# Performance work log

Measured on AMD Instinct MI355X. Metric: run time of the kernel, lower is better.

## Reference

```python
import jax, jax.numpy as jnp
import numpy as np

GROUP_SIZE = 64  # int4 precision
QMAX = 7.0       # symmetric int4 quant scale divisor


def setup_inputs() -> dict:
    key = jax.random.key(0)
    ks = jax.random.split(key, 8)
    B, S, C_in, C_out, R = 1, 4096, 3072, 3072, 32
    G = C_in // GROUP_SIZE
    x = jax.random.normal(ks[0], (B, S, C_in), dtype=jnp.float32)
    # unpacked int4 weight codes in [0,16); reference subtracts 8 -> signed int4 [-8,7]
    qweight = jax.random.randint(ks[1], (C_out, C_in), 0, 16, dtype=jnp.int32)
    # small positive per-group, per-out-channel weight scales
    wscales = jax.random.uniform(ks[2], (G, C_out), dtype=jnp.float32) * 0.01 + 0.001
    # positive smoothing factors bounded away from zero
    smooth_factor = jax.random.uniform(ks[3], (C_in,), dtype=jnp.float32) + 0.5
    proj_down = jax.random.normal(ks[4], (C_in, R), dtype=jnp.float32) * (1.0 / np.sqrt(C_in))
    proj_up = jax.random.normal(ks[5], (C_out, R), dtype=jnp.float32) * (1.0 / np.sqrt(R))
    bias = jax.random.normal(ks[6], (C_out,), dtype=jnp.float32) * 0.02
    return {
        "x": x,
        "qweight": qweight,
        "wscales": wscales,
        "smooth_factor": smooth_factor,
        "proj_down": proj_down,
        "proj_up": proj_up,
        "bias": bias,
    }


def reference(x, qweight, wscales, smooth_factor, proj_down, proj_up, bias):
    B, S, C = x.shape
    C_out = qweight.shape[0]
    M = B * S
    G = C // GROUP_SIZE

    # --- smoothing: x_hat = x / s (SVDQuant smoothing on activations) ---
    xs = x.reshape(M, C) / smooth_factor  # (M, C)

    # --- low-rank branch hidden state (fused with quantization in CUDA kernel) ---
    lora_act = jnp.einsum('mc,cr->mr', xs, proj_down)  # (M, R)

    # --- dynamic per-token, per-group int4 activation quantization ---
    xg = xs.reshape(M, G, GROUP_SIZE)
    amax = jnp.max(jnp.abs(xg), axis=-1, keepdims=True)          # (M, G, 1)
    ascale = amax / QMAX
    q = jnp.clip(jnp.round(xg / jnp.maximum(ascale, 1e-8)), -8.0, 7.0)
    x_dq = (q * ascale).reshape(M, C)                            # dequantized activations

    # --- weight dequantization: signed int4 codes * per-group/out-channel scales ---
    qw = qweight.astype(jnp.float32) - 8.0                       # (C_out, C) in [-8, 7]
    w_dq = (qw.reshape(C_out, G, GROUP_SIZE) * wscales.T[:, :, None]).reshape(C_out, C)

    # --- quantized GEMM + low-rank correction + bias ---
    out = jnp.einsum('mc,oc->mo', x_dq, w_dq)
    out = out + jnp.einsum('mr,or->mo', lora_act, proj_up) + bias
    return out.reshape(B, S, C_out)
```

## Files before the change

### kernel.cpp

```cpp
#include <hip/hip_runtime.h>
#include <stdint.h>

typedef unsigned short u16;

#define MTOK 4096
#define CIN  3072
#define COUT 3072
#define RANK 32
#define KT48 48
#define RS   3136
#define LKSPLIT 16
#define LKC (CIN/LKSPLIT)

#define LORA_BLK (MTOK/128*LKSPLIT)
#define WDQ_BLK COUT


typedef __attribute__((ext_vector_type(8))) short bf16x8;
typedef __attribute__((ext_vector_type(4))) float f32x4;

__device__ __forceinline__ u16 f2bf(float f) {
  union { float f; unsigned u; } v; v.f = f;
  unsigned r = v.u + 0x7FFFu + ((v.u >> 16) & 1u);
  return (u16)(r >> 16);
}

__device__ __forceinline__ void gload_lds16(const void* g, void* l) {
  __builtin_amdgcn_global_load_lds(
      (const __attribute__((address_space(1))) unsigned int*)g,
      (__attribute__((address_space(3))) unsigned int*)l, 16, 0, 0);
}

__device__ __forceinline__ float quant1(float xs, float ascale, float qd) {
  float q = rintf(xs / qd);
  q = fminf(fmaxf(q, -8.f), 7.f);
  return q * ascale;
}

__global__ __launch_bounds__(256) void prep_kernel(
    const float* __restrict__ x, const float* __restrict__ smooth,
    const int* __restrict__ qw, const float* __restrict__ wsc,
    const float* __restrict__ pd, const float* __restrict__ pu,
    u16* __restrict__ xdq, u16* __restrict__ wdq, u16* __restrict__ pu_bf,
    float* __restrict__ lp)
{
  const int b = blockIdx.x;
  const int t = threadIdx.x;

  if (b < LORA_BLK) {
    __shared__ __align__(16) u16 sA[128 * 64];
    __shared__ __align__(16) u16 sB[32 * 64];
    const int m0 = (b >> 4) * 128;
    const int kblk = b & 15;
    const int wave = t >> 6, lane = t & 63;
    const int lm = lane & 15, lkq = (lane >> 4) * 8;

    f32x4 acc[2][2];
    const f32x4 fz = {0.f, 0.f, 0.f, 0.f};
#pragma unroll
    for (int i = 0; i < 2; ++i)
#pragma unroll
      for (int j = 0; j < 2; ++j) acc[i][j] = fz;

    for (int kt = 0; kt < LKC / 64; ++kt) {
      const int k0 = kblk * LKC + kt * 64;
      const int col = (t & 15) * 4;
#pragma unroll
      for (int it = 0; it < 8; ++it) {
        const int row = it * 16 + (t >> 4);
        const float4 xv = *(const float4*)(x + (size_t)(m0 + row) * CIN + k0 + col);
        const float4 sv = *(const float4*)(smooth + k0 + col);
        const float xs0 = xv.x / sv.x, xs1 = xv.y / sv.y;
        const float xs2 = xv.z / sv.z, xs3 = xv.w / sv.w;
        ushort4 ov;
        ov.x = f2bf(xs0); ov.y = f2bf(xs1); ov.z = f2bf(xs2); ov.w = f2bf(xs3);
        *(ushort4*)&sA[row * 64 + col] = ov;
        float a = fmaxf(fmaxf(fabsf(xs0), fabsf(xs1)), fmaxf(fabsf(xs2), fabsf(xs3)));
#pragma unroll
        for (int off = 1; off < 16; off <<= 1) a = fmaxf(a, __shfl_xor(a, off));
        const float ascale = a / 7.0f;
        const float qd = fmaxf(ascale, 1e-8f);
        ushort4 oq;
        oq.x = f2bf(quant1(xs0, ascale, qd));
        oq.y = f2bf(quant1(xs1, ascale, qd));
        oq.z = f2bf(quant1(xs2, ascale, qd));
        oq.w = f2bf(quant1(xs3, ascale, qd));
        *(ushort4*)(xdq + (size_t)(m0 + row) * RS + k0 + col) = oq;
      }
#pragma unroll
      for (int i = 0; i < 8; ++i) {
        const int idx = i * 256 + t;
        const int k = idx >> 5, r = idx & 31;
        sB[r * 64 + k] = f2bf(pd[(size_t)(k0 + k) * RANK + r]);
      }
      __syncthreads();
#pragma unroll
      for (int kk = 0; kk < 2; ++kk) {
        const int ko = kk * 32 + lkq;
        bf16x8 af[2], bfr[2];
#pragma unroll
        for (int i = 0; i < 2; ++i)
          af[i] = *(const bf16x8*)&sA[(wave * 32 + i * 16 + lm) * 64 + ko];
#pragma unroll
        for (int j = 0; j < 2; ++j)
          bfr[j] = *(const bf16x8*)&sB[(j * 16 + lm) * 64 + ko];
#pragma unroll
        for (int i = 0; i < 2; ++i)
#pragma unroll
          for (int j = 0; j < 2; ++j)
            acc[i][j] = __builtin_amdgcn_mfma_f32_16x16x32_bf16(af[i], bfr[j], acc[i][j], 0, 0, 0);
      }
      __syncthreads();
    }
    float* lpk = lp + (size_t)kblk * MTOK * RANK;
#pragma unroll
    for (int i = 0; i < 2; ++i)
#pragma unroll
      for (int j = 0; j < 2; ++j) {
        const int col = j * 16 + lm;
        const int row0 = m0 + wave * 32 + i * 16 + (lane >> 4) * 4;
#pragma unroll
        for (int r = 0; r < 4; ++r)
          lpk[(size_t)(row0 + r) * RANK + col] = acc[i][j][r];
      }
  } else {
    const int o = b - LORA_BLK;
    const int4* qrow = (const int4*)(qw + (size_t)o * CIN);
    u16* orow = wdq + (size_t)o * RS;
#pragma unroll
    for (int p = 0; p < 3; ++p) {
      const int c4 = p * 256 + t;
      const int g = (c4 * 4) >> 6;
      const float ws = wsc[g * COUT + o];
      const int4 qv = qrow[c4];
      ushort4 ov;
      ov.x = f2bf((float)(qv.x - 8) * ws);
      ov.y = f2bf((float)(qv.y - 8) * ws);
      ov.z = f2bf((float)(qv.z - 8) * ws);
      ov.w = f2bf((float)(qv.w - 8) * ws);
      ((ushort4*)orow)[c4] = ov;
    }
    if (t < RANK) pu_bf[(size_t)o * RANK + t] = f2bf(pu[(size_t)o * RANK + t]);
  }
}

__global__ __launch_bounds__(256) void lora_fix_kernel(
    const float* __restrict__ lp, u16* __restrict__ lora_bf)
{
  const int idx = blockIdx.x * 256 + threadIdx.x;
  const int m = idx >> 5, c = idx & 31;
  float s = 0.f;
#pragma unroll
  for (int k = 0; k < LKSPLIT; ++k) s += lp[((size_t)k * MTOK + m) * RANK + c];
  lora_bf[(size_t)m * RANK + c] = f2bf(s);
}

__global__ __launch_bounds__(256) void gemm_kernel(
    const u16* __restrict__ xdq, const u16* __restrict__ wdq,
    const u16* __restrict__ pu_bf, const u16* __restrict__ lora_bf,
    const float* __restrict__ bias, float* __restrict__ out)
{
  __shared__ __align__(16) u16 sA[128 * 64];
  __shared__ __align__(16) u16 sB[128 * 64];
  const int t = threadIdx.x;
  const int wave = t >> 6, lane = t & 63;
  const int wm = wave >> 1, wn = wave & 1;
  const int m0 = blockIdx.y * 128, n0 = blockIdx.x * 128;
  const int lrow = lane >> 3;
  const int gcol = ((lane & 7) ^ lrow) * 8;

  f32x4 acc[4][4];
  const f32x4 fz = {0.f, 0.f, 0.f, 0.f};
#pragma unroll
  for (int i = 0; i < 4; ++i)
#pragma unroll
    for (int j = 0; j < 4; ++j) acc[i][j] = fz;

  const int lm = lane & 15;
  const int xs7 = lm & 7;
  const int q4 = lane >> 4;

  for (int kt = 0; kt < KT48; ++kt) {
    const u16* Ab = xdq + (size_t)m0 * RS + kt * 64;
    const u16* Bb = wdq + (size_t)n0 * RS + kt * 64;
#pragma unroll
    for (int r = 0; r < 4; ++r) {
      const int ci = wave * 4 + r;
      const int row = ci * 8 + lrow;
      gload_lds16(Ab + (size_t)row * RS + gcol, &sA[ci * 512 + lane * 8]);
      gload_lds16(Bb + (size_t)row * RS + gcol, &sB[ci * 512 + lane * 8]);
    }
    __syncthreads();
#pragma unroll
    for (int kk = 0; kk < 2; ++kk) {
      const int csw = ((kk * 4 + q4) ^ xs7) * 8;
      bf16x8 af[4], bfr[4];
#pragma unroll
      for (int i = 0; i < 4; ++i)
        af[i] = *(const bf16x8*)&sA[(wm * 64 + i * 16 + lm) * 64 + csw];
#pragma unroll
      for (int j = 0; j < 4; ++j)
        bfr[j] = *(const bf16x8*)&sB[(wn * 64 + j * 16 + lm) * 64 + csw];
#pragma unroll
      for (int i = 0; i < 4; ++i)
#pragma unroll
        for (int j = 0; j < 4; ++j)
          acc[i][j] = __builtin_amdgcn_mfma_f32_16x16x32_bf16(af[i], bfr[j], acc[i][j], 0, 0, 0);
    }
    __syncthreads();
  }

  bf16x8 afl[4], bfl[4];
#pragma unroll
  for (int i = 0; i < 4; ++i) {
    const int arow = m0 + wm * 64 + i * 16 + lm;
    afl[i] = *(const bf16x8*)(lora_bf + (size_t)arow * RANK + q4 * 8);
  }
#pragma unroll
  for (int j = 0; j < 4; ++j) {
    const int bcol = n0 + wn * 64 + j * 16 + lm;
    bfl[j] = *(const bf16x8*)(pu_bf + (size_t)bcol * RANK + q4 * 8);
  }
#pragma unroll
  for (int i = 0; i < 4; ++i)
#pragma unroll
    for (int j = 0; j < 4; ++j)
      acc[i][j] = __builtin_amdgcn_mfma_f32_16x16x32_bf16(afl[i], bfl[j], acc[i][j], 0, 0, 0);

#pragma unroll
  for (int j = 0; j < 4; ++j) {
    const int col = n0 + wn * 64 + j * 16 + lm;
    const float bv = bias[col];
#pragma unroll
    for (int i = 0; i < 4; ++i) {
      const int row0 = m0 + wm * 64 + i * 16 + (lane >> 4) * 4;
#pragma unroll
      for (int r = 0; r < 4; ++r)
        out[(size_t)(row0 + r) * COUT + col] = acc[i][j][r] + bv;
    }
  }
}

extern "C" void kernel_launch(void* const* d_in, const int* in_sizes, int n_in,
                              void* d_out, int out_size, void* d_ws, size_t ws_size,
                              hipStream_t stream) {
  const float* x      = (const float*)d_in[0];
  const int*   qw     = (const int*)d_in[1];
  const float* wsc    = (const float*)d_in[2];
  const float* smooth = (const float*)d_in[3];
  const float* pd     = (const float*)d_in[4];
  const float* pu     = (const float*)d_in[5];
  const float* bias   = (const float*)d_in[6];
  float* out = (float*)d_out;

  u16* xdq     = (u16*)d_ws;
  u16* wdq     = xdq + (size_t)MTOK * RS;
  u16* pu_bf   = wdq + (size_t)COUT * RS;
  u16* lora_bf = pu_bf + (size_t)COUT * RANK;
  float* lp    = (float*)(lora_bf + (size_t)MTOK * RANK);

  prep_kernel<<<LORA_BLK + WDQ_BLK, 256, 0, stream>>>(
      x, smooth, qw, wsc, pd, pu, xdq, wdq, pu_bf, lp);
  lora_fix_kernel<<<MTOK * RANK / 256, 256, 0, stream>>>(lp, lora_bf);
  gemm_kernel<<<dim3(COUT / 128, MTOK / 128), 256, 0, stream>>>(
      xdq, wdq, pu_bf, lora_bf, bias, out);
}
```

Measured before the change: 257.7 us.

## Rewrite bf16 GEMM as 256x256 tile, 8-wave, double-buffered LDS pipeline

The GEMM kernel moves from 128x128 tiles with 4 waves and a single LDS buffer to 256x256 tiles with 8 waves. It double-buffers the A and B halves in LDS and interleaves async global-to-LDS loads with MFMA phases, using explicit barriers, vmcnt waits and setprio. An XCD-aware block swizzle maps the 192 workgroups to tiles. The aim is to hide global load latency behind compute and raise arithmetic intensity per LDS byte, at the cost of heavy register pressure (128 accumulator vectors per thread) and fragile hand scheduling.

```diff
diff --git a/kernel.cpp b/kernel.cpp
--- a/kernel.cpp
+++ b/kernel.cpp
@@ -155,88 +155,158 @@
   lora_bf[(size_t)m * RANK + c] = f2bf(s);
 }
 
-__global__ __launch_bounds__(256) void gemm_kernel(
+
+__device__ __forceinline__ void stage_half(const u16* __restrict__ g, u16* lds_base,
+                                           int kt, int half, int buf, int t) {
+#pragma unroll
+  for (int r = 0; r < 2; ++r) {
+    const int ld = r * 512 + t;
+    const int row = ld >> 3;
+    const int d = ld & 7;
+    const int s0 = d ^ ((row >> 2) & 7);
+    const int c16 = ((s0 & 1) << 2) | (s0 >> 1);
+    gload_lds16(g + (size_t)(half * 128 + row) * RS + kt * 64 + c16 * 8,
+                lds_base + buf * 16384 + half * 8192 + ld * 8);
+  }
+}
+
+#define DSA(buf, mh) \
+  _Pragma("unroll") for (int i = 0; i < 4; ++i) { \
+    const int rl = wm * 64 + i * 16 + lm; \
+    _Pragma("unroll") for (int kk = 0; kk < 2; ++kk) \
+      af[i][kk] = *(const bf16x8*)&lds[(buf)*16384 + (mh)*8192 + rl * 64 + \
+                    ((((q4 << 1) | kk) ^ ((rl >> 2) & 7)) << 3)]; \
+  }
+
+#define DSB(buf, nh, BF) \
+  _Pragma("unroll") for (int j = 0; j < 2; ++j) { \
+    const int rl = wn * 32 + j * 16 + lm; \
+    _Pragma("unroll") for (int kk = 0; kk < 2; ++kk) \
+      BF[j][kk] = *(const bf16x8*)&lds[32768 + (buf)*16384 + (nh)*8192 + rl * 64 + \
+                    ((((q4 << 1) | kk) ^ ((rl >> 2) & 7)) << 3)]; \
+  }
+
+#define MFMA_Q(mh, nh, BF) \
+  __builtin_amdgcn_s_setprio(1); \
+  _Pragma("unroll") for (int i = 0; i < 4; ++i) \
+  _Pragma("unroll") for (int j = 0; j < 2; ++j) \
+  _Pragma("unroll") for (int kk = 0; kk < 2; ++kk) \
+    acc[(mh)*4 + i][(nh)*2 + j] = __builtin_amdgcn_mfma_f32_16x16x32_bf16( \
+        af[i][kk], BF[j][kk], acc[(mh)*4 + i][(nh)*2 + j], 0, 0, 0); \
+  __builtin_amdgcn_s_setprio(0);
+
+#define PH_OPEN() \
+  __builtin_amdgcn_sched_barrier(0); \
+  __builtin_amdgcn_s_barrier(); \
+  asm volatile("s_waitcnt lgkmcnt(0)" ::: "memory"); \
+  __builtin_amdgcn_sched_barrier(0)
+
+#define PH_CLOSE() \
+  __builtin_amdgcn_sched_barrier(0); \
+  __builtin_amdgcn_s_barrier(); \
+  __builtin_amdgcn_sched_barrier(0)
+
+#define VM4() asm volatile("s_waitcnt vmcnt(4)" ::: "memory")
+#define VM0() asm volatile("s_waitcnt vmcnt(0)" ::: "memory")
+
+#define TILE8(cur, S0, S1, S2, S3, VMI) do { \
+  DSA(cur, 0); DSB(cur, 0, bf0); S0; \
+  PH_OPEN(); MFMA_Q(0, 0, bf0); PH_CLOSE(); \
+  DSB(cur, 1, bf1); S1; \
+  PH_OPEN(); MFMA_Q(0, 1, bf1); PH_CLOSE(); \
+  DSA(cur, 1); S2; \
+  PH_OPEN(); MFMA_Q(1, 1, bf1); PH_CLOSE(); \
+  S3; \
+  PH_OPEN(); MFMA_Q(1, 0, bf0); VMI; PH_CLOSE(); \
+} while (0)
+
+__global__ __launch_bounds__(512, 2) void gemm_kernel(
     const u16* __restrict__ xdq, const u16* __restrict__ wdq,
     const u16* __restrict__ pu_bf, const u16* __restrict__ lora_bf,
     const float* __restrict__ bias, float* __restrict__ out)
 {
-  __shared__ __align__(16) u16 sA[128 * 64];
-  __shared__ __align__(16) u16 sB[128 * 64];
+  __shared__ __align__(16) u16 lds[65536];
+
   const int t = threadIdx.x;
-  const int wave = t >> 6, lane = t & 63;
-  const int wm = wave >> 1, wn = wave & 1;
-  const int m0 = blockIdx.y * 128, n0 = blockIdx.x * 128;
-  const int lrow = lane >> 3;
-  const int gcol = ((lane & 7) ^ lrow) * 8;
-
-  f32x4 acc[4][4];
+  const int wid = t >> 6, lane = t & 63;
+  const int wm = wid >> 2, wn = wid & 3;
+  const int lm = lane & 15, q4 = lane >> 4;
+
+  const int wg = blockIdx.x;
+  const int swz = (wg & 7) * 24 + (wg >> 3);
+  const int by = swz / 12, bx = swz % 12;
+  const int m0 = by * 256, n0 = bx * 256;
+
+  const u16* Ag = xdq + (size_t)m0 * RS;
+  const u16* Bg = wdq + (size_t)n0 * RS;
+  u16* ldsB = lds + 32768;
+
+  f32x4 acc[8][4];
   const f32x4 fz = {0.f, 0.f, 0.f, 0.f};
 #pragma unroll
-  for (int i = 0; i < 4; ++i)
+  for (int i = 0; i < 8; ++i)
 #pragma unroll
     for (int j = 0; j < 4; ++j) acc[i][j] = fz;
 
-  const int lm = lane & 15;
-  const int xs7 = lm & 7;
-  const int q4 = lane >> 4;
-
-  for (int kt = 0; kt < KT48; ++kt) {
-    const u16* Ab = xdq + (size_t)m0 * RS + kt * 64;
-    const u16* Bb = wdq + (size_t)n0 * RS + kt * 64;
-#pragma unroll
-    for (int r = 0; r < 4; ++r) {
-      const int ci = wave * 4 + r;
-      const int row = ci * 8 + lrow;
-      gload_lds16(Ab + (size_t)row * RS + gcol, &sA[ci * 512 + lane * 8]);
-      gload_lds16(Bb + (size_t)row * RS + gcol, &sB[ci * 512 + lane * 8]);
-    }
-    __syncthreads();
-#pragma unroll
-    for (int kk = 0; kk < 2; ++kk) {
-      const int csw = ((kk * 4 + q4) ^ xs7) * 8;
-      bf16x8 af[4], bfr[4];
-#pragma unroll
-      for (int i = 0; i < 4; ++i)
-        af[i] = *(const bf16x8*)&sA[(wm * 64 + i * 16 + lm) * 64 + csw];
-#pragma unroll
-      for (int j = 0; j < 4; ++j)
-        bfr[j] = *(const bf16x8*)&sB[(wn * 64 + j * 16 + lm) * 64 + csw];
-#pragma unroll
-      for (int i = 0; i < 4; ++i)
-#pragma unroll
-        for (int j = 0; j < 4; ++j)
-          acc[i][j] = __builtin_amdgcn_mfma_f32_16x16x32_bf16(af[i], bfr[j], acc[i][j], 0, 0, 0);
-    }
-    __syncthreads();
-  }
-
-  bf16x8 afl[4], bfl[4];
-#pragma unroll
-  for (int i = 0; i < 4; ++i) {
-    const int arow = m0 + wm * 64 + i * 16 + lm;
-    afl[i] = *(const bf16x8*)(lora_bf + (size_t)arow * RANK + q4 * 8);
-  }
-#pragma unroll
-  for (int j = 0; j < 4; ++j) {
-    const int bcol = n0 + wn * 64 + j * 16 + lm;
-    bfl[j] = *(const bf16x8*)(pu_bf + (size_t)bcol * RANK + q4 * 8);
-  }
-#pragma unroll
-  for (int i = 0; i < 4; ++i)
-#pragma unroll
-    for (int j = 0; j < 4; ++j)
-      acc[i][j] = __builtin_amdgcn_mfma_f32_16x16x32_bf16(afl[i], bfl[j], acc[i][j], 0, 0, 0);
-
-#pragma unroll
-  for (int j = 0; j < 4; ++j) {
-    const int col = n0 + wn * 64 + j * 16 + lm;
+  bf16x8 af[4][2], bf0[2][2], bf1[2][2];
+
+  stage_half(Ag, lds,  0, 0, 0, t);
+  stage_half(Bg, ldsB, 0, 0, 0, t);
+  stage_half(Ag, lds,  0, 1, 0, t);
+  stage_half(Bg, ldsB, 0, 1, 0, t);
+  stage_half(Ag, lds,  1, 0, 1, t);
+  stage_half(Bg, ldsB, 1, 1, 1, t);
+  VM4();
+  __builtin_amdgcn_s_barrier();
+  __builtin_amdgcn_sched_barrier(0);
+
+  for (int T = 0; T < 46; T += 2) {
+    TILE8(0,
+          stage_half(Ag, lds,  T + 1, 1, 1, t),
+          stage_half(Bg, ldsB, T + 1, 0, 1, t),
+          stage_half(Ag, lds,  T + 2, 0, 0, t),
+          stage_half(Bg, ldsB, T + 2, 1, 0, t),
+          VM4());
+    TILE8(1,
+          stage_half(Ag, lds,  T + 2, 1, 0, t),
+          stage_half(Bg, ldsB, T + 2, 0, 0, t),
+          stage_half(Ag, lds,  T + 3, 0, 1, t),
+          stage_half(Bg, ldsB, T + 3, 1, 1, t),
+          VM4());
+  }
+  TILE8(0,
+        stage_half(Ag, lds,  47, 1, 1, t),
+        stage_half(Bg, ldsB, 47, 0, 1, t),
+        (void)0,
+        (void)0,
+        VM0());
+  TILE8(1, (void)0, (void)0, (void)0, (void)0, (void)0);
+
+  bf16x8 bl[4];
+#pragma unroll
+  for (int b = 0; b < 4; ++b) {
+    const int bcol = n0 + (b >> 1) * 128 + wn * 32 + (b & 1) * 16 + lm;
+    bl[b] = *(const bf16x8*)(pu_bf + (size_t)bcol * RANK + q4 * 8);
+  }
+#pragma unroll
+  for (int a = 0; a < 8; ++a) {
+    const int arow = m0 + (a >> 2) * 128 + wm * 64 + (a & 3) * 16 + lm;
+    const bf16x8 al = *(const bf16x8*)(lora_bf + (size_t)arow * RANK + q4 * 8);
+#pragma unroll
+    for (int b = 0; b < 4; ++b)
+      acc[a][b] = __builtin_amdgcn_mfma_f32_16x16x32_bf16(al, bl[b], acc[a][b], 0, 0, 0);
+  }
+
+#pragma unroll
+  for (int b = 0; b < 4; ++b) {
+    const int col = n0 + (b >> 1) * 128 + wn * 32 + (b & 1) * 16 + lm;
     const float bv = bias[col];
 #pragma unroll
-    for (int i = 0; i < 4; ++i) {
-      const int row0 = m0 + wm * 64 + i * 16 + (lane >> 4) * 4;
+    for (int a = 0; a < 8; ++a) {
+      const int row0 = m0 + (a >> 2) * 128 + wm * 64 + (a & 3) * 16 + q4 * 4;
 #pragma unroll
       for (int r = 0; r < 4; ++r)
-        out[(size_t)(row0 + r) * COUT + col] = acc[i][j][r] + bv;
+        out[(size_t)(row0 + r) * COUT + col] = acc[a][b][r] + bv;
     }
   }
 }
@@ -262,6 +332,6 @@
   prep_kernel<<<LORA_BLK + WDQ_BLK, 256, 0, stream>>>(
       x, smooth, qw, wsc, pd, pu, xdq, wdq, pu_bf, lp);
   lora_fix_kernel<<<MTOK * RANK / 256, 256, 0, stream>>>(lp, lora_bf);
-  gemm_kernel<<<dim3(COUT / 128, MTOK / 128), 256, 0, stream>>>(
+  gemm_kernel<<<192, 512, 0, stream>>>(
       xdq, wdq, pu_bf, lora_bf, bias, out);
 }
```

New measurement: 257.9 us. No clear change (+0.1%).

## Rewrite GEMM with 256x256 tiles, triple-buffered LDS pipeline and 32x32 MFMA

Applied to the files above, without the earlier changes.

The bf16 GEMM moves from 128x128 tiles with a single LDS buffer and two syncs per k-step to 256x256 tiles on 512 threads. It uses a three-stage LDS ring with global_load_lds prefetch two tiles ahead, explicit vmcnt waits, and register double-buffered fragment reads that overlap the MFMA issue. It also switches to 32x32x16 MFMA, adds wave priority hints, and remaps workgroups across the 192-block grid for L2 locality. The aim is to hide global load latency and cut barrier overhead, at the cost of larger register and LDS use (96KB), possibly limiting occupancy.

```diff
diff --git a/kernel.cpp b/kernel.cpp
--- a/kernel.cpp
+++ b/kernel.cpp
@@ -7,17 +7,17 @@
 #define CIN  3072
 #define COUT 3072
 #define RANK 32
-#define KT48 48
 #define RS   3136
 #define LKSPLIT 16
 #define LKC (CIN/LKSPLIT)
+#define KTILES 96
 
 #define LORA_BLK (MTOK/128*LKSPLIT)
 #define WDQ_BLK COUT
 
-
 typedef __attribute__((ext_vector_type(8))) short bf16x8;
 typedef __attribute__((ext_vector_type(4))) float f32x4;
+typedef __attribute__((ext_vector_type(16))) float f32x16;
 
 __device__ __forceinline__ u16 f2bf(float f) {
   union { float f; unsigned u; } v; v.f = f;
@@ -155,88 +155,140 @@
   lora_bf[(size_t)m * RANK + c] = f2bf(s);
 }
 
-__global__ __launch_bounds__(256) void gemm_kernel(
+
+__device__ __forceinline__ void stage_tile(const u16* __restrict__ gA,
+                                           const u16* __restrict__ gB,
+                                           u16* ldsbuf, int kt, int t) {
+#pragma unroll
+  for (int r = 0; r < 2; ++r) {
+    const int id = r * 512 + t;
+    const int row = id >> 2;
+    const int l = id & 3;
+    const int src = l ^ ((row >> 1) & 3);
+    gload_lds16(gA + (size_t)row * RS + kt * 32 + src * 8, ldsbuf + id * 8);
+    gload_lds16(gB + (size_t)row * RS + kt * 32 + src * 8, ldsbuf + 8192 + id * 8);
+  }
+}
+
+#define RD_A(DST, BUF, S) \
+  _Pragma("unroll") for (int i_ = 0; i_ < 4; ++i_) { \
+    const int rr = wm * 128 + i_ * 32 + l31; \
+    const int ph = (((S) << 1) | hi) ^ ((rr >> 1) & 3); \
+    DST[i_] = *(const bf16x8*)&lds[(BUF) * 16384 + rr * 32 + ph * 8]; \
+  }
+
+#define RD_B(DST, BUF, S) \
+  _Pragma("unroll") for (int j_ = 0; j_ < 2; ++j_) { \
+    const int rr = wn * 64 + j_ * 32 + l31; \
+    const int ph = (((S) << 1) | hi) ^ ((rr >> 1) & 3); \
+    DST[j_] = *(const bf16x8*)&lds[(BUF) * 16384 + 8192 + rr * 32 + ph * 8]; \
+  }
+
+#define MM(A_, B_) \
+  __builtin_amdgcn_s_setprio(1); \
+  _Pragma("unroll") for (int i_ = 0; i_ < 4; ++i_) \
+  _Pragma("unroll") for (int j_ = 0; j_ < 2; ++j_) \
+    acc[i_][j_] = __builtin_amdgcn_mfma_f32_32x32x16_bf16(A_[i_], B_[j_], acc[i_][j_], 0, 0, 0); \
+  __builtin_amdgcn_s_setprio(0);
+
+#define VM4() asm volatile("s_waitcnt vmcnt(4)" ::: "memory")
+#define VM0() asm volatile("s_waitcnt vmcnt(0)" ::: "memory")
+
+#define TILE(T_, CB, NB, SB, DOSTAGE, DONEXT, VMW) do { \
+  if (DOSTAGE) stage_tile(Ag, Bg, lds + (SB) * 16384, (T_) + 2, tid); \
+  __builtin_amdgcn_sched_barrier(0); \
+  RD_A(aQ, CB, 1); RD_B(bQ, CB, 1); \
+  __builtin_amdgcn_sched_barrier(0); \
+  MM(aP, bP); \
+  __builtin_amdgcn_sched_barrier(0); \
+  VMW; \
+  if (DONEXT) { \
+    __builtin_amdgcn_s_barrier(); \
+    __builtin_amdgcn_sched_barrier(0); \
+    RD_A(aP, NB, 0); RD_B(bP, NB, 0); \
+    __builtin_amdgcn_sched_barrier(0); \
+  } \
+  MM(aQ, bQ); \
+  __builtin_amdgcn_sched_barrier(0); \
+} while (0)
+
+__global__ __launch_bounds__(512, 2) void gemm_kernel(
     const u16* __restrict__ xdq, const u16* __restrict__ wdq,
     const u16* __restrict__ pu_bf, const u16* __restrict__ lora_bf,
     const float* __restrict__ bias, float* __restrict__ out)
 {
-  __shared__ __align__(16) u16 sA[128 * 64];
-  __shared__ __align__(16) u16 sB[128 * 64];
-  const int t = threadIdx.x;
-  const int wave = t >> 6, lane = t & 63;
-  const int wm = wave >> 1, wn = wave & 1;
-  const int m0 = blockIdx.y * 128, n0 = blockIdx.x * 128;
-  const int lrow = lane >> 3;
-  const int gcol = ((lane & 7) ^ lrow) * 8;
-
-  f32x4 acc[4][4];
-  const f32x4 fz = {0.f, 0.f, 0.f, 0.f};
+  __shared__ __align__(16) u16 lds[49152];
+
+  const int tid = threadIdx.x;
+  const int wid = tid >> 6, lane = tid & 63;
+  const int wm = wid >> 2, wn = wid & 3;
+  const int l31 = lane & 31, hi = lane >> 5;
+
+  const int wg = blockIdx.x;
+  const int swz = (wg & 7) * 24 + (wg >> 3);
+  const int by = swz / 12, bx = swz % 12;
+  const int m0 = by * 256, n0 = bx * 256;
+
+  const u16* Ag = xdq + (size_t)m0 * RS;
+  const u16* Bg = wdq + (size_t)n0 * RS;
+
+  f32x16 acc[4][2];
 #pragma unroll
   for (int i = 0; i < 4; ++i)
 #pragma unroll
-    for (int j = 0; j < 4; ++j) acc[i][j] = fz;
-
-  const int lm = lane & 15;
-  const int xs7 = lm & 7;
-  const int q4 = lane >> 4;
-
-  for (int kt = 0; kt < KT48; ++kt) {
-    const u16* Ab = xdq + (size_t)m0 * RS + kt * 64;
-    const u16* Bb = wdq + (size_t)n0 * RS + kt * 64;
-#pragma unroll
-    for (int r = 0; r < 4; ++r) {
-      const int ci = wave * 4 + r;
-      const int row = ci * 8 + lrow;
-      gload_lds16(Ab + (size_t)row * RS + gcol, &sA[ci * 512 + lane * 8]);
-      gload_lds16(Bb + (size_t)row * RS + gcol, &sB[ci * 512 + lane * 8]);
-    }
-    __syncthreads();
-#pragma unroll
-    for (int kk = 0; kk < 2; ++kk) {
-      const int csw = ((kk * 4 + q4) ^ xs7) * 8;
-      bf16x8 af[4], bfr[4];
-#pragma unroll
-      for (int i = 0; i < 4; ++i)
-        af[i] = *(const bf16x8*)&sA[(wm * 64 + i * 16 + lm) * 64 + csw];
-#pragma unroll
-      for (int j = 0; j < 4; ++j)
-        bfr[j] = *(const bf16x8*)&sB[(wn * 64 + j * 16 + lm) * 64 + csw];
-#pragma unroll
-      for (int i = 0; i < 4; ++i)
-#pragma unroll
-        for (int j = 0; j < 4; ++j)
-          acc[i][j] = __builtin_amdgcn_mfma_f32_16x16x32_bf16(af[i], bfr[j], acc[i][j], 0, 0, 0);
-    }
-    __syncthreads();
-  }
-
-  bf16x8 afl[4], bfl[4];
-#pragma unroll
-  for (int i = 0; i < 4; ++i) {
-    const int arow = m0 + wm * 64 + i * 16 + lm;
-    afl[i] = *(const bf16x8*)(lora_bf + (size_t)arow * RANK + q4 * 8);
-  }
-#pragma unroll
-  for (int j = 0; j < 4; ++j) {
-    const int bcol = n0 + wn * 64 + j * 16 + lm;
-    bfl[j] = *(const bf16x8*)(pu_bf + (size_t)bcol * RANK + q4 * 8);
-  }
-#pragma unroll
-  for (int i = 0; i < 4; ++i)
-#pragma unroll
-    for (int j = 0; j < 4; ++j)
-      acc[i][j] = __builtin_amdgcn_mfma_f32_16x16x32_bf16(afl[i], bfl[j], acc[i][j], 0, 0, 0);
-
-#pragma unroll
-  for (int j = 0; j < 4; ++j) {
-    const int col = n0 + wn * 64 + j * 16 + lm;
+    for (int j = 0; j < 2; ++j) acc[i][j] = (f32x16)(0.0f);
+
+  bf16x8 aP[4], bP[2], aQ[4], bQ[2];
+
+  stage_tile(Ag, Bg, lds, 0, tid);
+  stage_tile(Ag, Bg, lds + 16384, 1, tid);
+  VM4();
+  __builtin_amdgcn_s_barrier();
+  __builtin_amdgcn_sched_barrier(0);
+  RD_A(aP, 0, 0); RD_B(bP, 0, 0);
+  __builtin_amdgcn_sched_barrier(0);
+
+  for (int T = 0; T < 93; T += 3) {
+    TILE(T + 0, 0, 1, 2, 1, 1, VM4());
+    TILE(T + 1, 1, 2, 0, 1, 1, VM4());
+    TILE(T + 2, 2, 0, 1, 1, 1, VM4());
+  }
+  TILE(93, 0, 1, 2, 1, 1, VM4());
+  TILE(94, 1, 2, 0, 0, 1, VM0());
+  TILE(95, 2, 0, 1, 0, 0, (void)0);
+
+#pragma unroll
+  for (int ks = 0; ks < 2; ++ks) {
+    bf16x8 bl[2], al[4];
+#pragma unroll
+    for (int j = 0; j < 2; ++j) {
+      const int col = n0 + wn * 64 + j * 32 + l31;
+      bl[j] = *(const bf16x8*)(pu_bf + (size_t)col * RANK + ks * 16 + hi * 8);
+    }
+#pragma unroll
+    for (int i = 0; i < 4; ++i) {
+      const int arow = m0 + wm * 128 + i * 32 + l31;
+      al[i] = *(const bf16x8*)(lora_bf + (size_t)arow * RANK + ks * 16 + hi * 8);
+    }
+#pragma unroll
+    for (int i = 0; i < 4; ++i)
+#pragma unroll
+      for (int j = 0; j < 2; ++j)
+        acc[i][j] = __builtin_amdgcn_mfma_f32_32x32x16_bf16(al[i], bl[j], acc[i][j], 0, 0, 0);
+  }
+
+#pragma unroll
+  for (int j = 0; j < 2; ++j) {
+    const int col = n0 + wn * 64 + j * 32 + l31;
     const float bv = bias[col];
 #pragma unroll
     for (int i = 0; i < 4; ++i) {
-      const int row0 = m0 + wm * 64 + i * 16 + (lane >> 4) * 4;
-#pragma unroll
-      for (int r = 0; r < 4; ++r)
-        out[(size_t)(row0 + r) * COUT + col] = acc[i][j][r] + bv;
+      const int rbase = m0 + wm * 128 + i * 32 + 4 * hi;
+#pragma unroll
+      for (int reg = 0; reg < 16; ++reg) {
+        const int row = rbase + (reg & 3) + 8 * (reg >> 2);
+        out[(size_t)row * COUT + col] = acc[i][j][reg] + bv;
+      }
     }
   }
 }
@@ -262,6 +314,6 @@
   prep_kernel<<<LORA_BLK + WDQ_BLK, 256, 0, stream>>>(
       x, smooth, qw, wsc, pd, pu, xdq, wdq, pu_bf, lp);
   lora_fix_kernel<<<MTOK * RANK / 256, 256, 0, stream>>>(lp, lora_bf);
-  gemm_kernel<<<dim3(COUT / 128, MTOK / 128), 256, 0, stream>>>(
+  gemm_kernel<<<192, 512, 0, stream>>>(
       xdq, wdq, pu_bf, lora_bf, bias, out);
 }
```

After: 226.1 us. 12.3% less time.
